# Kernel tuning notes

Measured on AMD Instinct MI355X. Metric: run time of the kernel, lower is better.

Reference implementation:

```python
import jax, jax.numpy as jnp
import numpy as np
from jax import lax

SAMPLE_RATE = 44100.0

def _shelf_coeffs(gain_db, fc, q, sr, high):
    # RBJ cookbook shelf biquad; high=True -> high_shelf, else low_shelf
    A = 10.0 ** (gain_db / 40.0)
    w0 = 2.0 * jnp.pi * (fc / sr)
    alpha = jnp.sin(w0) / (2.0 * q)
    c = jnp.cos(w0)
    sA = jnp.sqrt(A)
    sgn = 1.0 if high else -1.0
    b0 = A * (A + 1 + sgn * (A - 1) * c + 2 * sA * alpha)
    b1 = -2.0 * sgn * A * (A - 1 + sgn * (A + 1) * c)
    b2 = A * (A + 1 + sgn * (A - 1) * c - 2 * sA * alpha)
    a0 = A + 1 - sgn * (A - 1) * c + 2 * sA * alpha
    a1 = 2.0 * sgn * (A - 1 - sgn * (A + 1) * c)
    a2 = A + 1 - sgn * (A - 1) * c - 2 * sA * alpha
    b = jnp.stack([b0, b1, b2]) / a0
    a = jnp.stack([a0, a1, a2]) / a0
    return b, a

def _peaking_coeffs(gain_db, fc, q, sr):
    A = 10.0 ** (gain_db / 40.0)
    w0 = 2.0 * jnp.pi * (fc / sr)
    alpha = jnp.sin(w0) / (2.0 * q)
    c = jnp.cos(w0)
    b0 = 1 + alpha * A
    b1 = -2.0 * c
    b2 = 1 - alpha * A
    a0 = 1 + alpha / A
    a1 = -2.0 * c
    a2 = 1 - alpha / A
    b = jnp.stack([b0, b1, b2]) / a0
    a = jnp.stack([a0, a1, a2]) / a0
    return b, a

def _biquad_lfilter(b, a, x):
    # scipy.signal.lfilter with zero initial conditions, transposed DF-II.
    # x: (chs, T); state s: (chs, 2)
    b0, b1, b2 = b[0], b[1], b[2]
    a1, a2 = a[1], a[2]
    def step(s, xn):  # xn: (chs,)
        s1, s2 = s[:, 0], s[:, 1]
        yn = b0 * xn + s1
        s1n = b1 * xn - a1 * yn + s2
        s2n = b2 * xn - a2 * yn
        return jnp.stack([s1n, s2n], axis=1), yn
    s0 = jnp.zeros((x.shape[0], 2), x.dtype)
    _, y = lax.scan(step, s0, x.T)  # y: (T, chs)
    return y.T

def setup_inputs() -> dict:
    key = jax.random.key(0)
    x = jax.random.normal(key, (8, 2097152), dtype=jnp.float32)
    # rows: [low_shelf, band1, band2, band3, high_shelf]; cols: [gain_db, cutoff_hz, Q]
    eq_params = jnp.array([
        [3.0, 100.0, 0.9],
        [-2.5, 400.0, 1.2],
        [4.0, 1000.0, 2.0],
        [-5.0, 4000.0, 0.7],
        [2.5, 12000.0, 0.707],
    ], dtype=jnp.float32)
    return {"x": x, "eq_params": eq_params}

def reference(x, eq_params):
    sr = SAMPLE_RATE
    # low shelf
    b, a = _shelf_coeffs(eq_params[0, 0], eq_params[0, 1], eq_params[0, 2], sr, high=False)
    y = _biquad_lfilter(b, a, x)
    # 3 peaking bands
    for i in range(1, 4):
        b, a = _peaking_coeffs(eq_params[i, 0], eq_params[i, 1], eq_params[i, 2], sr)
        y = _biquad_lfilter(b, a, y)
    # high shelf
    b, a = _shelf_coeffs(eq_params[4, 0], eq_params[4, 1], eq_params[4, 2], sr, high=True)
    y = _biquad_lfilter(b, a, y)
    return y.astype(jnp.float32)
```

## Files before the change

kernel.cpp:

```cpp
#include <hip/hip_runtime.h>

#define SRATE 44100.0
#define L_CHUNK 256
#define SAMPLES_PER_CH 2097152
#define CHUNKS_PER_CH 8192
#define NCH 8
#define TOTAL_CHUNKS 65536
#define NBLK 256
#define BLK_PER_CH 32
#define NWIN 16
#define WIN 16
#define STRIDE 17

#ifndef M_PI
#define M_PI 3.14159265358979323846
#endif

struct CoefD { double b0, b1, b2, a1, a2; };

__device__ void cascade_step_d(const CoefD* cf, double* s, double x) {
    double u = x;
    #pragma unroll
    for (int i = 0; i < 5; i++) {
        double y   = cf[i].b0 * u + s[2*i];
        double s1n = cf[i].b1 * u - cf[i].a1 * y + s[2*i+1];
        double s2n = cf[i].b2 * u - cf[i].a2 * y;
        s[2*i]   = s1n;
        s[2*i+1] = s2n;
        u = y;
    }
}

__global__ __launch_bounds__(128) void k0_setup(const float* __restrict__ eqp,
                                                float* __restrict__ coef_f,
                                                float* __restrict__ mats_f) {
    __shared__ CoefD cf[5];
    __shared__ double M[100];
    int t = threadIdx.x;

    if (t == 0) {
        for (int i = 0; i < 5; i++) {
            double g  = (double)eqp[i*3 + 0];
            double fc = (double)eqp[i*3 + 1];
            double q  = (double)eqp[i*3 + 2];
            double A  = pow(10.0, g / 40.0);
            double w0 = 2.0 * M_PI * (fc / SRATE);
            double al = sin(w0) / (2.0 * q);
            double c  = cos(w0);
            double b0, b1, b2, a0, a1, a2;
            if (i == 0 || i == 4) {
                double sgn = (i == 4) ? 1.0 : -1.0;
                double sA = sqrt(A);
                b0 = A * ((A + 1.0) + sgn * (A - 1.0) * c + 2.0 * sA * al);
                b1 = -2.0 * sgn * A * ((A - 1.0) + sgn * (A + 1.0) * c);
                b2 = A * ((A + 1.0) + sgn * (A - 1.0) * c - 2.0 * sA * al);
                a0 = (A + 1.0) - sgn * (A - 1.0) * c + 2.0 * sA * al;
                a1 = 2.0 * sgn * ((A - 1.0) - sgn * (A + 1.0) * c);
                a2 = (A + 1.0) - sgn * (A - 1.0) * c - 2.0 * sA * al;
            } else {
                b0 = 1.0 + al * A; b1 = -2.0 * c; b2 = 1.0 - al * A;
                a0 = 1.0 + al / A; a1 = -2.0 * c; a2 = 1.0 - al / A;
            }
            cf[i].b0 = b0 / a0; cf[i].b1 = b1 / a0; cf[i].b2 = b2 / a0;
            cf[i].a1 = a1 / a0; cf[i].a2 = a2 / a0;
            coef_f[i*5 + 0] = (float)(b0 / a0);
            coef_f[i*5 + 1] = (float)(b1 / a0);
            coef_f[i*5 + 2] = (float)(b2 / a0);
            coef_f[i*5 + 3] = (float)(a1 / a0);
            coef_f[i*5 + 4] = (float)(a2 / a0);
        }
    }
    __syncthreads();

    if (t < 10) {
        double s[10];
        for (int k = 0; k < 10; k++) s[k] = (k == t) ? 1.0 : 0.0;
        cascade_step_d(cf, s, 0.0);
        for (int r = 0; r < 10; r++) M[r*10 + t] = s[r];
    }
    __syncthreads();

    for (int k = 1; k <= 20; k++) {
        double val = 0.0;
        if (t < 100) {
            int r = t / 10, c = t % 10;
            for (int j = 0; j < 10; j++) val += M[r*10 + j] * M[j*10 + c];
        }
        __syncthreads();
        if (t < 100) {
            M[t] = val;
            if (k >= 8 && k <= 15)  mats_f[(k-8)*100 + t]        = (float)val;
            if (k >= 16)            mats_f[800 + (k-16)*100 + t] = (float)val;
        }
        __syncthreads();
    }
}

__global__ __launch_bounds__(256) void k1_partial(const float* __restrict__ x,
                                                  const float* __restrict__ coef,
                                                  float* __restrict__ cbuf) {
    __shared__ float inb[2][256 * STRIDE];
    int t = threadIdx.x, b = blockIdx.x;

    float cb0[5], cb1[5], cb2[5], ca1[5], ca2[5];
    #pragma unroll
    for (int i = 0; i < 5; i++) {
        cb0[i] = coef[i*5+0]; cb1[i] = coef[i*5+1]; cb2[i] = coef[i*5+2];
        ca1[i] = coef[i*5+3]; ca2[i] = coef[i*5+4];
    }
    const float4* x4 = (const float4*)x;
    const size_t base4 = (size_t)b * 16384;
    const int cb = t >> 2, q = t & 3;

    float4 rr[4];
    #pragma unroll
    for (int k = 0; k < 4; k++)
        rr[k] = x4[base4 + (size_t)(cb + 64*k) * 64 + q];
    #pragma unroll
    for (int k = 0; k < 4; k++) {
        int o = (cb + 64*k) * STRIDE + q*4;
        inb[0][o+0] = rr[k].x; inb[0][o+1] = rr[k].y;
        inb[0][o+2] = rr[k].z; inb[0][o+3] = rr[k].w;
    }
    __syncthreads();

    float s[10];
    #pragma unroll
    for (int k = 0; k < 10; k++) s[k] = 0.0f;

    for (int w = 0; w < NWIN; w++) {
        if (w + 1 < NWIN) {
            #pragma unroll
            for (int k = 0; k < 4; k++)
                rr[k] = x4[base4 + (size_t)(cb + 64*k) * 64 + (w+1)*4 + q];
        }
        const float* cur = inb[w & 1] + t * STRIDE;
        #pragma unroll
        for (int i = 0; i < WIN; i++) {
            float u = cur[i];
            #pragma unroll
            for (int st = 0; st < 5; st++) {
                float y  = fmaf(cb0[st], u, s[2*st]);
                float t1 = fmaf(cb1[st], u, s[2*st+1]);
                s[2*st+1] = fmaf(-ca2[st], y, cb2[st] * u);
                s[2*st]   = fmaf(-ca1[st], y, t1);
                u = y;
            }
        }
        __syncthreads();
        if (w + 1 < NWIN) {
            float* nb = inb[(w+1) & 1];
            #pragma unroll
            for (int k = 0; k < 4; k++) {
                int o = (cb + 64*k) * STRIDE + q*4;
                nb[o+0] = rr[k].x; nb[o+1] = rr[k].y;
                nb[o+2] = rr[k].z; nb[o+3] = rr[k].w;
            }
        }
        __syncthreads();
    }
    #pragma unroll
    for (int r = 0; r < 10; r++)
        cbuf[(size_t)b * 2560 + r * 256 + t] = s[r];
}

__global__ __launch_bounds__(256) void k2a_scan(const float* __restrict__ mats_f,
                                                const float* __restrict__ cbuf,
                                                float* __restrict__ ibuf,
                                                float* __restrict__ abuf) {
    __shared__ float Mds[800];
    __shared__ float buf[256][11];
    int t = threadIdx.x, b = blockIdx.x;

    for (int i = t; i < 800; i += 256) Mds[i] = mats_f[i];

    float v[10];
    #pragma unroll
    for (int r = 0; r < 10; r++) {
        v[r] = cbuf[(size_t)b * 2560 + r * 256 + t];
        buf[t][r] = v[r];
    }
    __syncthreads();

    for (int d = 0; d < 8; d++) {
        float nv[10];
        bool act = (t >= (1 << d));
        if (act) {
            int src = t - (1 << d);
            #pragma unroll
            for (int r = 0; r < 10; r++) {
                float acc = v[r];
                #pragma unroll
                for (int k = 0; k < 10; k++)
                    acc = fmaf(Mds[d*100 + r*10 + k], buf[src][k], acc);
                nv[r] = acc;
            }
        }
        __syncthreads();
        if (act) {
            #pragma unroll
            for (int r = 0; r < 10; r++) { v[r] = nv[r]; buf[t][r] = nv[r]; }
        }
        __syncthreads();
    }

    #pragma unroll
    for (int r = 0; r < 10; r++)
        ibuf[(size_t)b * 2560 + r * 256 + t] = (t > 0) ? buf[t-1][r] : 0.0f;
    if (t == 255) {
        #pragma unroll
        for (int r = 0; r < 10; r++) abuf[b * 10 + r] = v[r];
    }
}

__global__ __launch_bounds__(256) void k2b_scan(const float* __restrict__ mats_f,
                                                const float* __restrict__ abuf,
                                                float* __restrict__ bbuf) {
    __shared__ float Qds[500];
    __shared__ float buf[256][11];
    int t = threadIdx.x;
    int i = t & 31;

    for (int k = t; k < 500; k += 256) Qds[k] = mats_f[800 + k];

    float v[10];
    #pragma unroll
    for (int r = 0; r < 10; r++) { v[r] = abuf[t * 10 + r]; buf[t][r] = v[r]; }
    __syncthreads();

    for (int e = 0; e < 5; e++) {
        float nv[10];
        bool act = (i >= (1 << e));
        if (act) {
            int src = t - (1 << e);
            #pragma unroll
            for (int r = 0; r < 10; r++) {
                float acc = v[r];
                #pragma unroll
                for (int k = 0; k < 10; k++)
                    acc = fmaf(Qds[e*100 + r*10 + k], buf[src][k], acc);
                nv[r] = acc;
            }
        }
        __syncthreads();
        if (act) {
            #pragma unroll
            for (int r = 0; r < 10; r++) { v[r] = nv[r]; buf[t][r] = nv[r]; }
        }
        __syncthreads();
    }
    #pragma unroll
    for (int r = 0; r < 10; r++)
        bbuf[t * 10 + r] = (i > 0) ? buf[t-1][r] : 0.0f;
}

__global__ __launch_bounds__(256) void k3_final(const float* __restrict__ x,
                                                const float* __restrict__ coef,
                                                const float* __restrict__ mats_f,
                                                const float* __restrict__ ibuf,
                                                const float* __restrict__ bbuf,
                                                float* __restrict__ out) {
    __shared__ float inb[2][256 * STRIDE];
    __shared__ float outb[256 * STRIDE];
    __shared__ float Mds[800];
    int t = threadIdx.x, b = blockIdx.x;

    const float4* x4 = (const float4*)x;
    float4* o4 = (float4*)out;
    const size_t base4 = (size_t)b * 16384;
    const int cb = t >> 2, q = t & 3;

    float4 rr[4];
    #pragma unroll
    for (int k = 0; k < 4; k++)
        rr[k] = x4[base4 + (size_t)(cb + 64*k) * 64 + q];

    for (int i = t; i < 800; i += 256) Mds[i] = mats_f[i];

    float cb0[5], cb1[5], cb2[5], ca1[5], ca2[5];
    #pragma unroll
    for (int i = 0; i < 5; i++) {
        cb0[i] = coef[i*5+0]; cb1[i] = coef[i*5+1]; cb2[i] = coef[i*5+2];
        ca1[i] = coef[i*5+3]; ca2[i] = coef[i*5+4];
    }

    float s[10];
    #pragma unroll
    for (int r = 0; r < 10; r++)
        s[r] = ibuf[(size_t)b * 2560 + r * 256 + t];

    float v[10];
    #pragma unroll
    for (int r = 0; r < 10; r++) v[r] = bbuf[b * 10 + r];

    #pragma unroll
    for (int k = 0; k < 4; k++) {
        int o = (cb + 64*k) * STRIDE + q*4;
        inb[0][o+0] = rr[k].x; inb[0][o+1] = rr[k].y;
        inb[0][o+2] = rr[k].z; inb[0][o+3] = rr[k].w;
    }
    __syncthreads();

    for (int d = 0; d < 8; d++) {
        float wv[10];
        #pragma unroll
        for (int r = 0; r < 10; r++) {
            float acc = 0.0f;
            #pragma unroll
            for (int k = 0; k < 10; k++)
                acc = fmaf(Mds[d*100 + r*10 + k], v[k], acc);
            wv[r] = acc;
        }
        bool bit = (t >> d) & 1;
        #pragma unroll
        for (int r = 0; r < 10; r++) v[r] = bit ? wv[r] : v[r];
    }
    #pragma unroll
    for (int r = 0; r < 10; r++) s[r] += v[r];

    for (int w = 0; w < NWIN; w++) {
        if (w + 1 < NWIN) {
            #pragma unroll
            for (int k = 0; k < 4; k++)
                rr[k] = x4[base4 + (size_t)(cb + 64*k) * 64 + (w+1)*4 + q];
        }
        const float* cur = inb[w & 1] + t * STRIDE;
        float* orow = outb + t * STRIDE;
        #pragma unroll
        for (int i = 0; i < WIN; i++) {
            float u = cur[i];
            #pragma unroll
            for (int st = 0; st < 5; st++) {
                float y  = fmaf(cb0[st], u, s[2*st]);
                float t1 = fmaf(cb1[st], u, s[2*st+1]);
                s[2*st+1] = fmaf(-ca2[st], y, cb2[st] * u);
                s[2*st]   = fmaf(-ca1[st], y, t1);
                u = y;
            }
            orow[i] = u;
        }
        __syncthreads();

        #pragma unroll
        for (int k = 0; k < 4; k++) {
            int o = (cb + 64*k) * STRIDE + q*4;
            float4 ov = make_float4(outb[o+0], outb[o+1], outb[o+2], outb[o+3]);
            o4[base4 + (size_t)(cb + 64*k) * 64 + (size_t)w*4 + q] = ov;
        }
        if (w + 1 < NWIN) {
            float* nb = inb[(w+1) & 1];
            #pragma unroll
            for (int k = 0; k < 4; k++) {
                int o = (cb + 64*k) * STRIDE + q*4;
                nb[o+0] = rr[k].x; nb[o+1] = rr[k].y;
                nb[o+2] = rr[k].z; nb[o+3] = rr[k].w;
            }
        }
        __syncthreads();
    }
}

extern "C" void kernel_launch(void* const* d_in, const int* in_sizes, int n_in,
                              void* d_out, int out_size, void* d_ws, size_t ws_size,
                              hipStream_t stream) {
    const float* x   = (const float*)d_in[0];
    const float* eqp = (const float*)d_in[1];
    float* out = (float*)d_out;
    char* ws = (char*)d_ws;

    float* coef_f = (float*)ws;
    float* mats_f = (float*)(ws + 256);
    float* cbuf   = (float*)(ws + 8192);
    float* ibuf   = (float*)(ws + 8192 + 2621440);
    float* abuf   = (float*)(ws + 8192 + 2*2621440);
    float* bbuf   = (float*)(ws + 8192 + 2*2621440 + 16384);

    hipLaunchKernelGGL(k0_setup, dim3(1), dim3(128), 0, stream, eqp, coef_f, mats_f);
    hipLaunchKernelGGL(k1_partial, dim3(NBLK), dim3(256), 0, stream, x, coef_f, cbuf);
    hipLaunchKernelGGL(k2a_scan, dim3(NBLK), dim3(256), 0, stream, mats_f, cbuf, ibuf, abuf);
    hipLaunchKernelGGL(k2b_scan, dim3(1), dim3(256), 0, stream, mats_f, abuf, bbuf);
    hipLaunchKernelGGL(k3_final, dim3(NBLK), dim3(256), 0, stream,
                       x, coef_f, mats_f, ibuf, bbuf, out);
}
```

Before: 170.8 us.

## Shrink chunks to 64 samples, fuse block scan into partial kernel

Each chunk shrinks from 256 to 64 samples, which quadruples the block count (1024) and the chunk count. The intra-block scan is folded into k1_partial, removing one launch and the cbuf round-trip through global memory. The cross-block scan grows to 1024 threads and 7 levels, and the precomputed matrix powers shift to match the shorter chunk. Shared-memory double buffering is replaced by a single buffer with an extra barrier, and a launch bound of 4 waves is added, trading less overlap for more parallelism and occupancy.

Measured after the change: 186.9 us. 1.09x slower.

```diff
diff --git a/kernel.cpp b/kernel.cpp
--- a/kernel.cpp
+++ b/kernel.cpp
@@ -1,14 +1,15 @@
 #include <hip/hip_runtime.h>
 
 #define SRATE 44100.0
-#define L_CHUNK 256
+#define L_CHUNK 64
 #define SAMPLES_PER_CH 2097152
-#define CHUNKS_PER_CH 8192
+#define CHUNKS_PER_CH 32768
 #define NCH 8
-#define TOTAL_CHUNKS 65536
-#define NBLK 256
-#define BLK_PER_CH 32
-#define NWIN 16
+#define TOTAL_CHUNKS 262144
+#define CPB 256
+#define NBLK 1024
+#define BLK_PER_CH 128
+#define NWIN 4
 #define WIN 16
 #define STRIDE 17
 
@@ -89,18 +90,32 @@
         __syncthreads();
         if (t < 100) {
             M[t] = val;
-            if (k >= 8 && k <= 15)  mats_f[(k-8)*100 + t]        = (float)val;
-            if (k >= 16)            mats_f[800 + (k-16)*100 + t] = (float)val;
-        }
-        __syncthreads();
-    }
-}
-
-__global__ __launch_bounds__(256) void k1_partial(const float* __restrict__ x,
-                                                  const float* __restrict__ coef,
-                                                  float* __restrict__ cbuf) {
-    __shared__ float inb[2][256 * STRIDE];
+            if (k >= 6 && k <= 13)  mats_f[(k-6)*100 + t]        = (float)val;
+            if (k >= 14)            mats_f[800 + (k-14)*100 + t] = (float)val;
+        }
+        __syncthreads();
+    }
+}
+
+__global__ __launch_bounds__(256, 4) void k1_partial(const float* __restrict__ x,
+                                                     const float* __restrict__ coef,
+                                                     const float* __restrict__ mats_f,
+                                                     float* __restrict__ ibuf,
+                                                     float* __restrict__ abuf) {
+    __shared__ float smem[CPB * STRIDE];
+    __shared__ float Mds[800];
     int t = threadIdx.x, b = blockIdx.x;
+
+    const float4* x4 = (const float4*)x;
+    const size_t base4 = (size_t)b * (CPB * L_CHUNK / 4);
+    const int cb = t >> 2, q = t & 3;
+
+    float4 rr[4];
+    #pragma unroll
+    for (int k = 0; k < 4; k++)
+        rr[k] = x4[base4 + (size_t)(cb + 64*k) * (L_CHUNK/4) + q];
+
+    for (int i = t; i < 800; i += 256) Mds[i] = mats_f[i];
 
     float cb0[5], cb1[5], cb2[5], ca1[5], ca2[5];
     #pragma unroll
@@ -108,19 +123,12 @@
         cb0[i] = coef[i*5+0]; cb1[i] = coef[i*5+1]; cb2[i] = coef[i*5+2];
         ca1[i] = coef[i*5+3]; ca2[i] = coef[i*5+4];
     }
-    const float4* x4 = (const float4*)x;
-    const size_t base4 = (size_t)b * 16384;
-    const int cb = t >> 2, q = t & 3;
-
-    float4 rr[4];
-    #pragma unroll
-    for (int k = 0; k < 4; k++)
-        rr[k] = x4[base4 + (size_t)(cb + 64*k) * 64 + q];
+
     #pragma unroll
     for (int k = 0; k < 4; k++) {
         int o = (cb + 64*k) * STRIDE + q*4;
-        inb[0][o+0] = rr[k].x; inb[0][o+1] = rr[k].y;
-        inb[0][o+2] = rr[k].z; inb[0][o+3] = rr[k].w;
+        smem[o+0] = rr[k].x; smem[o+1] = rr[k].y;
+        smem[o+2] = rr[k].z; smem[o+3] = rr[k].w;
     }
     __syncthreads();
 
@@ -132,9 +140,9 @@
         if (w + 1 < NWIN) {
             #pragma unroll
             for (int k = 0; k < 4; k++)
-                rr[k] = x4[base4 + (size_t)(cb + 64*k) * 64 + (w+1)*4 + q];
-        }
-        const float* cur = inb[w & 1] + t * STRIDE;
+                rr[k] = x4[base4 + (size_t)(cb + 64*k) * (L_CHUNK/4) + (w+1)*4 + q];
+        }
+        const float* cur = smem + t * STRIDE;
         #pragma unroll
         for (int i = 0; i < WIN; i++) {
             float u = cur[i];
@@ -149,37 +157,19 @@
         }
         __syncthreads();
         if (w + 1 < NWIN) {
-            float* nb = inb[(w+1) & 1];
             #pragma unroll
             for (int k = 0; k < 4; k++) {
                 int o = (cb + 64*k) * STRIDE + q*4;
-                nb[o+0] = rr[k].x; nb[o+1] = rr[k].y;
-                nb[o+2] = rr[k].z; nb[o+3] = rr[k].w;
-            }
-        }
-        __syncthreads();
-    }
-    #pragma unroll
-    for (int r = 0; r < 10; r++)
-        cbuf[(size_t)b * 2560 + r * 256 + t] = s[r];
-}
-
-__global__ __launch_bounds__(256) void k2a_scan(const float* __restrict__ mats_f,
-                                                const float* __restrict__ cbuf,
-                                                float* __restrict__ ibuf,
-                                                float* __restrict__ abuf) {
-    __shared__ float Mds[800];
-    __shared__ float buf[256][11];
-    int t = threadIdx.x, b = blockIdx.x;
-
-    for (int i = t; i < 800; i += 256) Mds[i] = mats_f[i];
+                smem[o+0] = rr[k].x; smem[o+1] = rr[k].y;
+                smem[o+2] = rr[k].z; smem[o+3] = rr[k].w;
+            }
+            __syncthreads();
+        }
+    }
 
     float v[10];
     #pragma unroll
-    for (int r = 0; r < 10; r++) {
-        v[r] = cbuf[(size_t)b * 2560 + r * 256 + t];
-        buf[t][r] = v[r];
-    }
+    for (int r = 0; r < 10; r++) { v[r] = s[r]; smem[t*11 + r] = v[r]; }
     __syncthreads();
 
     for (int d = 0; d < 8; d++) {
@@ -192,43 +182,43 @@
                 float acc = v[r];
                 #pragma unroll
                 for (int k = 0; k < 10; k++)
-                    acc = fmaf(Mds[d*100 + r*10 + k], buf[src][k], acc);
+                    acc = fmaf(Mds[d*100 + r*10 + k], smem[src*11 + k], acc);
                 nv[r] = acc;
             }
         }
         __syncthreads();
         if (act) {
             #pragma unroll
-            for (int r = 0; r < 10; r++) { v[r] = nv[r]; buf[t][r] = nv[r]; }
+            for (int r = 0; r < 10; r++) { v[r] = nv[r]; smem[t*11 + r] = nv[r]; }
         }
         __syncthreads();
     }
 
     #pragma unroll
     for (int r = 0; r < 10; r++)
-        ibuf[(size_t)b * 2560 + r * 256 + t] = (t > 0) ? buf[t-1][r] : 0.0f;
+        ibuf[(size_t)b * 2560 + r * 256 + t] = (t > 0) ? smem[(t-1)*11 + r] : 0.0f;
     if (t == 255) {
         #pragma unroll
         for (int r = 0; r < 10; r++) abuf[b * 10 + r] = v[r];
     }
 }
 
-__global__ __launch_bounds__(256) void k2b_scan(const float* __restrict__ mats_f,
-                                                const float* __restrict__ abuf,
-                                                float* __restrict__ bbuf) {
-    __shared__ float Qds[500];
-    __shared__ float buf[256][11];
+__global__ __launch_bounds__(1024) void k2b_scan(const float* __restrict__ mats_f,
+                                                 const float* __restrict__ abuf,
+                                                 float* __restrict__ bbuf) {
+    __shared__ float Qds[700];
+    __shared__ float buf[1024][11];
     int t = threadIdx.x;
-    int i = t & 31;
-
-    for (int k = t; k < 500; k += 256) Qds[k] = mats_f[800 + k];
+    int i = t & (BLK_PER_CH - 1);
+
+    for (int k = t; k < 700; k += 1024) Qds[k] = mats_f[800 + k];
 
     float v[10];
     #pragma unroll
     for (int r = 0; r < 10; r++) { v[r] = abuf[t * 10 + r]; buf[t][r] = v[r]; }
     __syncthreads();
 
-    for (int e = 0; e < 5; e++) {
+    for (int e = 0; e < 7; e++) {
         float nv[10];
         bool act = (i >= (1 << e));
         if (act) {
@@ -254,26 +244,26 @@
         bbuf[t * 10 + r] = (i > 0) ? buf[t-1][r] : 0.0f;
 }
 
-__global__ __launch_bounds__(256) void k3_final(const float* __restrict__ x,
-                                                const float* __restrict__ coef,
-                                                const float* __restrict__ mats_f,
-                                                const float* __restrict__ ibuf,
-                                                const float* __restrict__ bbuf,
-                                                float* __restrict__ out) {
-    __shared__ float inb[2][256 * STRIDE];
-    __shared__ float outb[256 * STRIDE];
+__global__ __launch_bounds__(256, 4) void k3_final(const float* __restrict__ x,
+                                                   const float* __restrict__ coef,
+                                                   const float* __restrict__ mats_f,
+                                                   const float* __restrict__ ibuf,
+                                                   const float* __restrict__ bbuf,
+                                                   float* __restrict__ out) {
+    __shared__ float inb[CPB * STRIDE];
+    __shared__ float outb[CPB * STRIDE];
     __shared__ float Mds[800];
     int t = threadIdx.x, b = blockIdx.x;
 
     const float4* x4 = (const float4*)x;
     float4* o4 = (float4*)out;
-    const size_t base4 = (size_t)b * 16384;
+    const size_t base4 = (size_t)b * (CPB * L_CHUNK / 4);
     const int cb = t >> 2, q = t & 3;
 
     float4 rr[4];
     #pragma unroll
     for (int k = 0; k < 4; k++)
-        rr[k] = x4[base4 + (size_t)(cb + 64*k) * 64 + q];
+        rr[k] = x4[base4 + (size_t)(cb + 64*k) * (L_CHUNK/4) + q];
 
     for (int i = t; i < 800; i += 256) Mds[i] = mats_f[i];
 
@@ -288,7 +278,6 @@
     #pragma unroll
     for (int r = 0; r < 10; r++)
         s[r] = ibuf[(size_t)b * 2560 + r * 256 + t];
-
     float v[10];
     #pragma unroll
     for (int r = 0; r < 10; r++) v[r] = bbuf[b * 10 + r];
@@ -296,8 +285,8 @@
     #pragma unroll
     for (int k = 0; k < 4; k++) {
         int o = (cb + 64*k) * STRIDE + q*4;
-        inb[0][o+0] = rr[k].x; inb[0][o+1] = rr[k].y;
-        inb[0][o+2] = rr[k].z; inb[0][o+3] = rr[k].w;
+        inb[o+0] = rr[k].x; inb[o+1] = rr[k].y;
+        inb[o+2] = rr[k].z; inb[o+3] = rr[k].w;
     }
     __syncthreads();
 
@@ -322,9 +311,9 @@
         if (w + 1 < NWIN) {
             #pragma unroll
             for (int k = 0; k < 4; k++)
-                rr[k] = x4[base4 + (size_t)(cb + 64*k) * 64 + (w+1)*4 + q];
-        }
-        const float* cur = inb[w & 1] + t * STRIDE;
+                rr[k] = x4[base4 + (size_t)(cb + 64*k) * (L_CHUNK/4) + (w+1)*4 + q];
+        }
+        const float* cur = inb + t * STRIDE;
         float* orow = outb + t * STRIDE;
         #pragma unroll
         for (int i = 0; i < WIN; i++) {
@@ -345,18 +334,17 @@
         for (int k = 0; k < 4; k++) {
             int o = (cb + 64*k) * STRIDE + q*4;
             float4 ov = make_float4(outb[o+0], outb[o+1], outb[o+2], outb[o+3]);
-            o4[base4 + (size_t)(cb + 64*k) * 64 + (size_t)w*4 + q] = ov;
+            o4[base4 + (size_t)(cb + 64*k) * (L_CHUNK/4) + (size_t)w*4 + q] = ov;
         }
         if (w + 1 < NWIN) {
-            float* nb = inb[(w+1) & 1];
             #pragma unroll
             for (int k = 0; k < 4; k++) {
                 int o = (cb + 64*k) * STRIDE + q*4;
-                nb[o+0] = rr[k].x; nb[o+1] = rr[k].y;
-                nb[o+2] = rr[k].z; nb[o+3] = rr[k].w;
-            }
-        }
-        __syncthreads();
+                inb[o+0] = rr[k].x; inb[o+1] = rr[k].y;
+                inb[o+2] = rr[k].z; inb[o+3] = rr[k].w;
+            }
+            __syncthreads();
+        }
     }
 }
 
@@ -370,15 +358,14 @@
 
     float* coef_f = (float*)ws;
     float* mats_f = (float*)(ws + 256);
-    float* cbuf   = (float*)(ws + 8192);
-    float* ibuf   = (float*)(ws + 8192 + 2621440);
-    float* abuf   = (float*)(ws + 8192 + 2*2621440);
-    float* bbuf   = (float*)(ws + 8192 + 2*2621440 + 16384);
+    float* abuf   = (float*)(ws + 8192);
+    float* bbuf   = (float*)(ws + 49152);
+    float* ibuf   = (float*)(ws + 98304);
 
     hipLaunchKernelGGL(k0_setup, dim3(1), dim3(128), 0, stream, eqp, coef_f, mats_f);
-    hipLaunchKernelGGL(k1_partial, dim3(NBLK), dim3(256), 0, stream, x, coef_f, cbuf);
-    hipLaunchKernelGGL(k2a_scan, dim3(NBLK), dim3(256), 0, stream, mats_f, cbuf, ibuf, abuf);
-    hipLaunchKernelGGL(k2b_scan, dim3(1), dim3(256), 0, stream, mats_f, abuf, bbuf);
+    hipLaunchKernelGGL(k1_partial, dim3(NBLK), dim3(256), 0, stream,
+                       x, coef_f, mats_f, ibuf, abuf);
+    hipLaunchKernelGGL(k2b_scan, dim3(1), dim3(1024), 0, stream, mats_f, abuf, bbuf);
     hipLaunchKernelGGL(k3_final, dim3(NBLK), dim3(256), 0, stream,
                        x, coef_f, mats_f, ibuf, bbuf, out);
 }
```
